# Kernel tuning notes

Hardware: AMD Instinct MI355X
Metric: run time of the kernel (lower is better)

## Reference

```python
import jax, jax.numpy as jnp
import numpy as np

B, IN_DIM, OUT_DIM, N, H = 64, 2, 1, 512, 64
SEQ, HOR, K, NSUP = 12, 12, 2, 2
TOT = 1 + NSUP * K  # number of diffusion matrices (identity + K steps per support)


def _lin_init(key, fan_in, shape):
    return jax.random.normal(key, shape, jnp.float32) / np.sqrt(fan_in)


def setup_inputs() -> dict:
    key = jax.random.key(0)
    ks = jax.random.split(key, 16)
    inputs = jax.random.normal(ks[0], (B, IN_DIM, N, SEQ), jnp.float32)
    A = jax.random.uniform(ks[1], (NSUP, N, N), jnp.float32)
    supports = A / A.sum(axis=2, keepdims=True)  # row-normalized transition matrices
    params = {}
    i = 2
    for pre, in0 in (('e', IN_DIM), ('d', OUT_DIM)):
        for l in range(2):
            cin = (in0 if l == 0 else H) + H
            params[f'{pre}{l}_wg'] = _lin_init(ks[i], TOT * cin, (TOT * cin, 2 * H)); i += 1
            params[f'{pre}{l}_bg'] = jnp.zeros((2 * H,), jnp.float32)
            params[f'{pre}{l}_wc'] = _lin_init(ks[i], TOT * cin, (TOT * cin, H)); i += 1
            params[f'{pre}{l}_bc'] = jnp.zeros((H,), jnp.float32)
    params['proj_w'] = _lin_init(ks[i], H, (OUT_DIM, H))
    params['proj_b'] = jnp.zeros((OUT_DIM,), jnp.float32)
    return {'inputs': inputs, 'supports': supports, **params}


def _gconv(x, h, supports, W, b):
    # x: (B,Cx,N), h: (B,H,N) -> (B,Dout,N)
    z = jnp.concatenate([x, h], axis=1)
    feats = [z]
    for s in range(NSUP):
        xk = z
        for _ in range(K):
            xk = jnp.einsum('nm,bcm->bcn', supports[s], xk)
            feats.append(xk)
    zf = jnp.concatenate(feats, axis=1)  # (B, TOT*C, N)
    return jnp.einsum('bcn,cd->bdn', zf, W) + b[None, :, None]


def _cell(x, h, supports, wg, bg, wc, bc):
    ru = jax.nn.sigmoid(_gconv(x, h, supports, wg, bg))
    r, u = jnp.split(ru, 2, axis=1)
    c = jnp.tanh(_gconv(x, r * h, supports, wc, bc))
    return u * h + (1.0 - u) * c


def _run(inputs, supports, p):
    h0 = jnp.zeros((B, H, N), jnp.float32)
    h1 = jnp.zeros((B, H, N), jnp.float32)

    def enc_step(carry, x):
        h0, h1 = carry
        h0 = _cell(x, h0, supports, p['e0_wg'], p['e0_bg'], p['e0_wc'], p['e0_bc'])
        h1 = _cell(h0, h1, supports, p['e1_wg'], p['e1_bg'], p['e1_wc'], p['e1_bc'])
        return (h0, h1), None

    xs = jnp.moveaxis(inputs, -1, 0)  # (SEQ,B,IN_DIM,N)
    (h0, h1), _ = jax.lax.scan(enc_step, (h0, h1), xs)

    go = jnp.zeros((B, OUT_DIM, N), jnp.float32)

    def dec_step(carry, _):
        x, h0, h1 = carry
        h0 = _cell(x, h0, supports, p['d0_wg'], p['d0_bg'], p['d0_wc'], p['d0_bc'])
        h1 = _cell(h0, h1, supports, p['d1_wg'], p['d1_bg'], p['d1_wc'], p['d1_bc'])
        y = jnp.einsum('bhn,oh->bon', h1, p['proj_w']) + p['proj_b'][None, :, None]
        return (y, h0, h1), y

    _, ys = jax.lax.scan(dec_step, (go, h0, h1), None, length=HOR)
    return jnp.moveaxis(ys, 0, -1)  # (B, OUT_DIM, N, HOR)


def reference(inputs, supports, e0_wg, e0_bg, e0_wc, e0_bc, e1_wg, e1_bg, e1_wc, e1_bc,
              d0_wg, d0_bg, d0_wc, d0_bc, d1_wg, d1_bg, d1_wc, d1_bc, proj_w, proj_b):
    p = dict(e0_wg=e0_wg, e0_bg=e0_bg, e0_wc=e0_wc, e0_bc=e0_bc,
             e1_wg=e1_wg, e1_bg=e1_bg, e1_wc=e1_wc, e1_bc=e1_bc,
             d0_wg=d0_wg, d0_bg=d0_bg, d0_wc=d0_wc, d0_bc=d0_bc,
             d1_wg=d1_wg, d1_bg=d1_bg, d1_wc=d1_wc, d1_bc=d1_bc,
             proj_w=proj_w, proj_b=proj_b)
    return _run(inputs, supports, p)
```

## Files before the change

kernel.cpp:

```cpp
#include <hip/hip_runtime.h>

#define B_ 64
#define N_ 512

typedef __attribute__((ext_vector_type(8))) short bf8_t;
typedef __attribute__((ext_vector_type(16))) float f16_t;
typedef __attribute__((ext_vector_type(4))) float f4v_t;

#define MFMA32(a, b, c) __builtin_amdgcn_mfma_f32_32x32x16_bf16(a, b, c, 0, 0, 0)

__device__ __forceinline__ ushort f2bf(float x) {
  union { float f; unsigned u; } v; v.f = x;
  unsigned r = v.u + 0x7FFFu + ((v.u >> 16) & 1u);
  return (ushort)(r >> 16);
}
__device__ __forceinline__ float bf2f(ushort h) {
  union { unsigned u; float f; } v; v.u = ((unsigned)h) << 16;
  return v.f;
}

__device__ __forceinline__ void gld16(const ushort* g, ushort* l) {
  __builtin_amdgcn_global_load_lds(
      (const __attribute__((address_space(1))) unsigned int*)(uintptr_t)g,
      (__attribute__((address_space(3))) unsigned int*)(uintptr_t)l,
      16, 0, 0);
}

__device__ __forceinline__ int xcd_logical(int nwg) {
  int lin = blockIdx.x + gridDim.x * (blockIdx.y + gridDim.y * blockIdx.z);
  return (lin & 7) * (nwg >> 3) + (lin >> 3);
}

__device__ __forceinline__ int swz32(int r) { return (r >> 1) & 3; }

template <int ROWS, int THREADS>
__device__ __forceinline__ void stage_tile2(const ushort* g, int lda, int k0,
                                            ushort* l, int tid) {
  constexpr int RT = (ROWS * 32) / (THREADS * 8);
#pragma unroll
  for (int q = 0; q < RT; ++q) {
    int e  = q * THREADS * 8 + tid * 8;
    int r  = e >> 5;
    int c8 = (e >> 3) & 3;
    int g8 = c8 ^ swz32(r);
    gld16(g + (size_t)r * lda + k0 + g8 * 8, l + e);
  }
}

__device__ __forceinline__ void core128(
    const ushort* Ah, const ushort* Al, int lda,
    const ushort* Bh, const ushort* Bl, int ldb,
    int K, ushort* lds, f16_t acc[2][2]) {
  constexpr int TILE = 128 * 32;
  constexpr int SSZ  = 4 * TILE;
  const int tid = threadIdx.x, lane = tid & 63, wave = tid >> 6;
  const int ar = lane & 31, hb = lane >> 5;
  const int wm = wave >> 1, wn = wave & 1;

  auto stage = [&](int buf, int k0) {
    ushort* lb = lds + buf * SSZ;
    stage_tile2<128, 256>(Ah, lda, k0, lb, tid);
    stage_tile2<128, 256>(Al, lda, k0, lb + TILE, tid);
    stage_tile2<128, 256>(Bh, ldb, k0, lb + 2 * TILE, tid);
    stage_tile2<128, 256>(Bl, ldb, k0, lb + 3 * TILE, tid);
  };

  const int nc = K >> 5;
  stage(0, 0);
  int buf = 0;
  for (int c = 0; c < nc; ++c) {
    __syncthreads();
    if (c + 1 < nc) stage(buf ^ 1, (c + 1) << 5);
    const ushort* lb = lds + buf * SSZ;
#pragma unroll
    for (int ks = 0; ks < 2; ++ks) {
      bf8_t ah[2], al[2], bh[2], bl[2];
#pragma unroll
      for (int i = 0; i < 2; ++i) {
        int r = wm * 64 + 32 * i + ar;
        int c8 = (ks * 2 + hb) ^ swz32(r);
        ah[i] = *(const bf8_t*)(lb + r * 32 + c8 * 8);
        al[i] = *(const bf8_t*)(lb + TILE + r * 32 + c8 * 8);
      }
#pragma unroll
      for (int j = 0; j < 2; ++j) {
        int r = wn * 64 + 32 * j + ar;
        int c8 = (ks * 2 + hb) ^ swz32(r);
        bh[j] = *(const bf8_t*)(lb + 2 * TILE + r * 32 + c8 * 8);
        bl[j] = *(const bf8_t*)(lb + 3 * TILE + r * 32 + c8 * 8);
      }
#pragma unroll
      for (int i = 0; i < 2; ++i)
#pragma unroll
        for (int j = 0; j < 2; ++j) {
          acc[i][j] = MFMA32(ah[i], bh[j], acc[i][j]);
          acc[i][j] = MFMA32(ah[i], bl[j], acc[i][j]);
          acc[i][j] = MFMA32(al[i], bh[j], acc[i][j]);
        }
    }
    buf ^= 1;
  }
}

__device__ __forceinline__ void core128_1(
    const ushort* Ah, int lda,
    const ushort* Bh, int ldb,
    int K, ushort* lds, f16_t acc[2][2]) {
  constexpr int TILE = 128 * 32;
  constexpr int SSZ  = 2 * TILE;
  const int tid = threadIdx.x, lane = tid & 63, wave = tid >> 6;
  const int ar = lane & 31, hb = lane >> 5;
  const int wm = wave >> 1, wn = wave & 1;

  auto stage = [&](int buf, int k0) {
    ushort* lb = lds + buf * SSZ;
    stage_tile2<128, 256>(Ah, lda, k0, lb, tid);
    stage_tile2<128, 256>(Bh, ldb, k0, lb + TILE, tid);
  };

  const int nc = K >> 5;
  stage(0, 0);
  int buf = 0;
  for (int c = 0; c < nc; ++c) {
    __syncthreads();
    if (c + 1 < nc) stage(buf ^ 1, (c + 1) << 5);
    const ushort* lb = lds + buf * SSZ;
#pragma unroll
    for (int ks = 0; ks < 2; ++ks) {
      bf8_t ah[2], bh[2];
#pragma unroll
      for (int i = 0; i < 2; ++i) {
        int r = wm * 64 + 32 * i + ar;
        int c8 = (ks * 2 + hb) ^ swz32(r);
        ah[i] = *(const bf8_t*)(lb + r * 32 + c8 * 8);
      }
#pragma unroll
      for (int j = 0; j < 2; ++j) {
        int r = wn * 64 + 32 * j + ar;
        int c8 = (ks * 2 + hb) ^ swz32(r);
        bh[j] = *(const bf8_t*)(lb + TILE + r * 32 + c8 * 8);
      }
#pragma unroll
      for (int i = 0; i < 2; ++i)
#pragma unroll
        for (int j = 0; j < 2; ++j)
          acc[i][j] = MFMA32(ah[i], bh[j], acc[i][j]);
    }
    buf ^= 1;
  }
}

__device__ __forceinline__ int crow32(int r, int hb) {
  return (r & 3) + 8 * (r >> 2) + 4 * hb;
}

__global__ __launch_bounds__(256) void stb_k(const float* __restrict__ S,
                                             ushort* __restrict__ Bcat,
                                             ushort* __restrict__ STb) {
  __shared__ float tile[16][17];
  int s = blockIdx.z;
  int n0 = blockIdx.y * 16, m0 = blockIdx.x * 16;
  int tx = threadIdx.x & 15, ty = threadIdx.x >> 4;
  float v = S[(size_t)s * 262144 + (size_t)(n0 + ty) * 512 + m0 + tx];
  tile[ty][tx] = v;
  Bcat[(size_t)(n0 + ty) * 2048 + (size_t)(2 * s) * 512 + m0 + tx] = f2bf(v);
  __syncthreads();
  STb[(size_t)s * 262144 + (size_t)(m0 + ty) * 512 + n0 + tx] = f2bf(tile[tx][ty]);
}

__global__ __launch_bounds__(256) void ssqm_k(const ushort* __restrict__ Bc,
                                              const ushort* __restrict__ STb,
                                              ushort* __restrict__ Bout) {
  __shared__ __attribute__((aligned(16))) ushort lds[2 * 2 * 128 * 32];
  int tid = threadIdx.x, lane = tid & 63, wave = tid >> 6;
  int wm = wave >> 1, wn = wave & 1, ar = lane & 31, hb = lane >> 5;
  int a = blockIdx.x, bm = blockIdx.y, s = blockIdx.z;
  f16_t acc[2][2] = {};
  core128_1(Bc + (size_t)(a * 128) * 2048 + (size_t)(2 * s) * 512, 2048,
            STb + (size_t)s * 262144 + (size_t)(bm * 128) * 512, 512,
            512, lds, acc);
#pragma unroll
  for (int i = 0; i < 2; ++i)
#pragma unroll
    for (int j = 0; j < 2; ++j) {
      int m_ = bm * 128 + wn * 64 + 32 * j + ar;
#pragma unroll
      for (int r = 0; r < 16; ++r) {
        int n_ = a * 128 + wm * 64 + 32 * i + crow32(r, hb);
        Bout[(size_t)n_ * 2048 + (size_t)(2 * s + 1) * 512 + m_] = f2bf(acc[i][j][r]);
      }
    }
}

struct WSrc { const float* wg[4]; const float* wc[4]; };

__global__ __launch_bounds__(256) void wprep_all_k(WSrc src,
                                                   ushort* __restrict__ Wbuf) {
  int idx = blockIdx.x * 256 + threadIdx.x;
  if (idx >= 4 * 147456) return;
  int ci = idx / 147456, r = idx % 147456;
  int C = (ci == 0) ? 66 : (ci == 2) ? 65 : 128;
  const float* WG = src.wg[ci];
  const float* WC = src.wc[ci];
  ushort v;
  if (r < 32768) {
    int e = r & 16383, c = e & 127, d = e >> 7;
    float x = (c < C) ? WG[(size_t)c * 128 + d] : 0.f;
    ushort hh = f2bf(x);
    v = (r < 16384) ? hh : f2bf(x - bf2f(hh));
  } else if (r < 98304) {
    int e = r - 32768, c = e & 127, i = e >> 7;
    int t = 1 + (i >> 7), d = i & 127;
    v = (c < C) ? f2bf(WG[(size_t)(t * C + c) * 128 + d]) : (ushort)0;
  } else if (r < 114688) {
    int e = (r - 98304) & 8191, c = e & 127, d = e >> 7;
    float x = (c < C) ? WC[(size_t)c * 64 + d] : 0.f;
    ushort hh = f2bf(x);
    v = (r < 106496) ? hh : f2bf(x - bf2f(hh));
  } else {
    int e = r - 114688, c = e & 127, i = e >> 7;
    int t = 1 + (i >> 6), d = i & 63;
    v = (c < C) ? f2bf(WC[(size_t)(t * C + c) * 64 + d]) : (ushort)0;
  }
  Wbuf[idx] = v;
}

__global__ __launch_bounds__(256) void packzT_k(const float* __restrict__ xsrc,
                                                int xmode, int t, int Cx, int C,
                                                const float* __restrict__ hT,
                                                ushort* __restrict__ Zh,
                                                ushort* __restrict__ Zl) {
  int jg = blockIdx.x * 256 + threadIdx.x;
  int b = jg >> 9, n = jg & 511;
  for (int c0 = 0; c0 < 128; c0 += 8) {
    bf8_t vh, vl;
#pragma unroll
    for (int q = 0; q < 8; ++q) {
      int c = c0 + q;
      float v;
      if (c < Cx) {
        if (xmode == 0)      v = xsrc[((size_t)(b * Cx + c) * 512 + n) * 12 + t];
        else if (xmode == 1) v = xsrc[jg];
        else                 v = xsrc[(size_t)jg * 64 + c];
      } else if (c < C) {
        v = hT[(size_t)jg * 64 + (c - Cx)];
      } else {
        v = 0.f;
      }
      ushort hh = f2bf(v);
      vh[q] = (short)hh;
      vl[q] = (short)f2bf(v - bf2f(hh));
    }
    *(bf8_t*)(Zh + (size_t)jg * 128 + c0) = vh;
    *(bf8_t*)(Zl + (size_t)jg * 128 + c0) = vl;
  }
}

template <int MODE>
__global__ __launch_bounds__(256, 2) void g1_k(const ushort* __restrict__ Wih,
                                               const ushort* __restrict__ Wil,
                                               const ushort* __restrict__ Wd,
                                               const ushort* __restrict__ Zh,
                                               const ushort* __restrict__ Zl,
                                               ushort* __restrict__ Gh,
                                               float* __restrict__ G0T, int K) {
  __shared__ __attribute__((aligned(16))) ushort lds[2 * 4 * 128 * 32];
  constexpr int DR = (MODE == 0) ? 128 : 64;
  constexpr int NMT = (MODE == 0) ? 4 : 2;
  int tid = threadIdx.x, lane = tid & 63, wave = tid >> 6;
  int wm = wave >> 1, wn = wave & 1, ar = lane & 31, hb = lane >> 5;
  int L = xcd_logical(256 * (NMT + 1));
  int mt = L % (NMT + 1), nt = L / (NMT + 1);
  f16_t acc[2][2] = {};
  if (mt == NMT) {
    core128(Wih, Wil, 128,
            Zh + (size_t)nt * 128 * 128, Zl + (size_t)nt * 128 * 128, 128,
            K, lds, acc);
#pragma unroll
    for (int i = 0; i < 2; ++i)
#pragma unroll
      for (int j = 0; j < 2; ++j) {
        int jg = nt * 128 + wn * 64 + 32 * j + ar;
#pragma unroll
        for (int r = 0; r < 16; ++r) {
          int d = wm * 64 + 32 * i + crow32(r, hb);
          if (d >= DR) continue;
          G0T[(size_t)jg * DR + d] = acc[i][j][r];
        }
      }
  } else {
    core128_1(Wd + (size_t)mt * 128 * 128, 128,
              Zh + (size_t)nt * 128 * 128, 128,
              K, lds, acc);
#pragma unroll
    for (int i = 0; i < 2; ++i)
#pragma unroll
      for (int j = 0; j < 2; ++j) {
        int jg = nt * 128 + wn * 64 + 32 * j + ar;
        int b = jg >> 9, m = jg & 511;
#pragma unroll
        for (int r = 0; r < 16; ++r) {
          int ii = mt * 128 + wm * 64 + 32 * i + crow32(r, hb);
          int tt = ii / DR, d = ii % DR;
          Gh[((size_t)(b * DR + d)) * 2048 + (size_t)tt * 512 + m] = f2bf(acc[i][j][r]);
        }
      }
  }
}

__global__ __launch_bounds__(256, 3) void ru1g_k(const ushort* __restrict__ Gh,
                                                 const ushort* __restrict__ Bch,
                                                 float* __restrict__ P) {
  __shared__ __attribute__((aligned(16))) ushort lds[2 * 2 * 128 * 32];
  int tid = threadIdx.x, lane = tid & 63, wave = tid >> 6;
  int wm = wave >> 1, wn = wave & 1, ar = lane & 31, hb = lane >> 5;
  int L = xcd_logical(768);
  int mt = L & 3, nt = (L >> 2) & 63, kz = L >> 8;
  int k0 = kz * 768;
  int K  = (kz == 2) ? 512 : 768;
  f16_t acc[2][2] = {};
  core128_1(Bch + (size_t)mt * 128 * 2048 + k0, 2048,
            Gh + (size_t)nt * 128 * 2048 + k0, 2048,
            K, lds, acc);
  float* Pz = P + (size_t)kz * 4194304;
#pragma unroll
  for (int i = 0; i < 2; ++i)
#pragma unroll
    for (int j = 0; j < 2; ++j) {
      int R = nt * 128 + wn * 64 + 32 * j + ar;
      int b = R >> 7, d = R & 127;
#pragma unroll
      for (int r = 0; r < 16; ++r) {
        int node = mt * 128 + wm * 64 + 32 * i + crow32(r, hb);
        Pz[((size_t)b * 512 + node) * 128 + d] = acc[i][j][r];
      }
    }
}

__global__ __launch_bounds__(256) void ru1f_k(const float* __restrict__ P,
                                              const float* __restrict__ G0T,
                                              const float* __restrict__ bg,
                                              const float* __restrict__ hT,
                                              float* __restrict__ U,
                                              ushort* __restrict__ Zh,
                                              ushort* __restrict__ Zl, int Cx) {
  int i4 = blockIdx.x * 256 + threadIdx.x;
  if (i4 >= 1048576) return;
  int base = i4 * 4;
  int row = base >> 7, d = base & 127;
  f4v_t p0 = *(const f4v_t*)(P + base);
  f4v_t p1 = *(const f4v_t*)(P + 4194304 + base);
  f4v_t p2 = *(const f4v_t*)(P + 2 * 4194304 + base);
  f4v_t g0 = *(const f4v_t*)(G0T + base);
  if (d < 64) {
    f4v_t hv = *(const f4v_t*)(hT + (size_t)row * 64 + d);
#pragma unroll
    for (int e = 0; e < 4; ++e) {
      float s = 1.f / (1.f + expf(-(p0[e] + p1[e] + p2[e] + g0[e] + bg[d + e])));
      float rh = s * hv[e];
      ushort hh = f2bf(rh);
      Zh[(size_t)row * 128 + Cx + d + e] = hh;
      Zl[(size_t)row * 128 + Cx + d + e] = f2bf(rh - bf2f(hh));
    }
  } else {
    f4v_t uo;
#pragma unroll
    for (int e = 0; e < 4; ++e)
      uo[e] = 1.f / (1.f + expf(-(p0[e] + p1[e] + p2[e] + g0[e] + bg[d + e])));
    *(f4v_t*)(U + (size_t)row * 64 + (d - 64)) = uo;
  }
}

__global__ __launch_bounds__(256, 3) void ru2g_k(const ushort* __restrict__ Gh,
                                                 const ushort* __restrict__ Bch,
                                                 float* __restrict__ P) {
  __shared__ __attribute__((aligned(16))) ushort lds[2 * 2 * 128 * 32];
  int tid = threadIdx.x, lane = tid & 63, wave = tid >> 6;
  int wm = wave >> 1, wn = wave & 1, ar = lane & 31, hb = lane >> 5;
  int L = xcd_logical(512);
  int mt = L & 3, nt = (L >> 2) & 31, kz = L >> 7;
  f16_t acc[2][2] = {};
  core128_1(Bch + (size_t)mt * 128 * 2048 + kz * 512, 2048,
            Gh + (size_t)nt * 128 * 2048 + kz * 512, 2048,
            512, lds, acc);
  float* Pz = P + (size_t)kz * 2097152;
#pragma unroll
  for (int i = 0; i < 2; ++i)
#pragma unroll
    for (int j = 0; j < 2; ++j) {
      int R = nt * 128 + wn * 64 + 32 * j + ar;
      int b = R >> 6, d = R & 63;
#pragma unroll
      for (int r = 0; r < 16; ++r) {
        int node = mt * 128 + wm * 64 + 32 * i + crow32(r, hb);
        Pz[((size_t)b * 512 + node) * 64 + d] = acc[i][j][r];
      }
    }
}

__global__ __launch_bounds__(256) void ru2f_k(const float* __restrict__ P,
                                              const float* __restrict__ G0c,
                                              const float* __restrict__ bc,
                                              const float* __restrict__ U,
                                              float* __restrict__ hT) {
  int i4 = blockIdx.x * 256 + threadIdx.x;
  if (i4 >= 524288) return;
  int base = i4 * 4;
  int d = base & 63;
  f4v_t p0 = *(const f4v_t*)(P + base);
  f4v_t p1 = *(const f4v_t*)(P + 2097152 + base);
  f4v_t p2 = *(const f4v_t*)(P + 2 * 2097152 + base);
  f4v_t p3 = *(const f4v_t*)(P + 3 * 2097152 + base);
  f4v_t g0 = *(const f4v_t*)(G0c + base);
  f4v_t uv = *(const f4v_t*)(U + base);
  f4v_t hv = *(const f4v_t*)(hT + base);
#pragma unroll
  for (int e = 0; e < 4; ++e) {
    float ct = tanhf(p0[e] + p1[e] + p2[e] + p3[e] + g0[e] + bc[d + e]);
    hv[e] = uv[e] * hv[e] + (1.f - uv[e]) * ct;
  }
  *(f4v_t*)(hT + base) = hv;
}

__global__ __launch_bounds__(256) void proj_out_k(const float* __restrict__ h1T,
                                                  const float* __restrict__ pw,
                                                  const float* __restrict__ pb,
                                                  float* __restrict__ ybuf,
                                                  float* __restrict__ out, int k) {
  int idx = blockIdx.x * blockDim.x + threadIdx.x;
  if (idx >= B_ * N_) return;
  float s = pb[0];
  const float* hrow = h1T + (size_t)idx * 64;
#pragma unroll
  for (int j = 0; j < 64; ++j)
    s = fmaf(pw[j], hrow[j], s);
  ybuf[idx] = s;
  out[(size_t)idx * 12 + k] = s;
}

extern "C" void kernel_launch(void* const* d_in, const int* in_sizes, int n_in,
                              void* d_out, int out_size, void* d_ws, size_t ws_size,
                              hipStream_t stream) {
  const float* inputs   = (const float*)d_in[0];
  const float* supports = (const float*)d_in[1];
  WSrc wsrc;
  wsrc.wg[0] = (const float*)d_in[2];  wsrc.wg[1] = (const float*)d_in[6];
  wsrc.wg[2] = (const float*)d_in[10]; wsrc.wg[3] = (const float*)d_in[14];
  wsrc.wc[0] = (const float*)d_in[4];  wsrc.wc[1] = (const float*)d_in[8];
  wsrc.wc[2] = (const float*)d_in[12]; wsrc.wc[3] = (const float*)d_in[16];
  const float* Bg[4] = { (const float*)d_in[3],  (const float*)d_in[7],
                         (const float*)d_in[11], (const float*)d_in[15] };
  const float* Bc[4] = { (const float*)d_in[5],  (const float*)d_in[9],
                         (const float*)d_in[13], (const float*)d_in[17] };
  const float* proj_w = (const float*)d_in[18];
  const float* proj_b = (const float*)d_in[19];
  float* out = (float*)d_out;

  char* p = (char*)d_ws;
  auto carve = [&](size_t bytes) { void* q = p; p += (bytes + 255) & ~(size_t)255; return q; };
  ushort* Bch  = (ushort*)carve((size_t)512 * 2048 * 2);
  ushort* zTh  = (ushort*)carve((size_t)32768 * 128 * 2);
  ushort* zTl  = (ushort*)carve((size_t)32768 * 128 * 2);
  ushort* Gh   = (ushort*)carve((size_t)8192 * 2048 * 2);
  float*  G0T  = (float*)carve((size_t)32768 * 128 * 4);
  float*  P    = (float*)carve((size_t)3 * 4194304 * 4);
  float*  U    = (float*)carve((size_t)2097152 * 4);
  float*  h0   = (float*)carve((size_t)2097152 * 4);
  float*  h1   = (float*)carve((size_t)2097152 * 4);
  float*  ybuf = (float*)carve((size_t)B_ * N_ * 4);
  ushort* Wbuf = (ushort*)carve((size_t)4 * 147456 * 2);
  ushort* STb  = (ushort*)U;

  hipMemsetAsync(h0, 0, (size_t)2097152 * 4 * 2 + (size_t)B_ * N_ * 4, stream);

  stb_k<<<dim3(32, 32, 2), 256, 0, stream>>>(supports, Bch, STb);
  ssqm_k<<<dim3(4, 4, 2), 256, 0, stream>>>(Bch, STb, Bch);
  wprep_all_k<<<(4 * 147456 + 255) / 256, 256, 0, stream>>>(wsrc, Wbuf);

  auto cell = [&](int ci, int Cx, const float* x, int xmode, int t, float* h) {
    int C = Cx + 64;
    int K1 = (C + 31) & ~31;
    ushort* cw = Wbuf + (size_t)ci * 147456;
    ushort* Wgid_h = cw;          ushort* Wgid_l = cw + 16384;
    ushort* Wgd    = cw + 32768;
    ushort* Wcid_h = cw + 98304;  ushort* Wcid_l = cw + 106496;
    ushort* Wcd    = cw + 114688;
    packzT_k<<<128, 256, 0, stream>>>(x, xmode, t, Cx, C, h, zTh, zTl);
    g1_k<0><<<dim3(256, 5), 256, 0, stream>>>(Wgid_h, Wgid_l, Wgd, zTh, zTl, Gh, G0T, K1);
    ru1g_k<<<dim3(64, 4, 3), 256, 0, stream>>>(Gh, Bch, P);
    ru1f_k<<<4096, 256, 0, stream>>>(P, G0T, Bg[ci], h, U, zTh, zTl, Cx);
    g1_k<1><<<dim3(256, 3), 256, 0, stream>>>(Wcid_h, Wcid_l, Wcd, zTh, zTl, Gh, G0T, K1);
    ru2g_k<<<dim3(32, 4, 4), 256, 0, stream>>>(Gh, Bch, P);
    ru2f_k<<<2048, 256, 0, stream>>>(P, G0T, Bc[ci], U, h);
  };

  for (int t = 0; t < 12; ++t) {
    cell(0, 2, inputs, 0, t, h0);
    cell(1, 64, h0, 2, 0, h1);
  }
  for (int k = 0; k < 12; ++k) {
    cell(2, 1, ybuf, 1, 0, h0);
    cell(3, 64, h0, 2, 0, h1);
    proj_out_k<<<(B_ * N_ + 255) / 256, 256, 0, stream>>>(h1, proj_w, proj_b, ybuf, out, k);
  }
}
```

Measured before the change: 6.206 ms.

## Fuse diffusion GEMMs with gate epilogues, dropping split-K partial buffers

Replaces the split-K GEMMs (ru1g/ru2g), which wrote fp32 partial sums to a P buffer, and their separate elementwise finalize kernels with single fused kernels. Each fused kernel runs the full K=2048 reduction and applies sigmoid/tanh and the GRU update in the epilogue. The GEMM core is templated over tile shapes, and smaller tiles (64x128, 64x64) are used so 512 blocks still fill the GPU without split-K. This removes large partial-sum traffic and two launches per cell. In exchange each block runs a longer serial K loop, and the epilogue does scattered, uncoalesced fp32 loads and stores.

After: 6.500 ms. +4.7%, slower.

```diff
diff --git a/kernel.cpp b/kernel.cpp
--- a/kernel.cpp
+++ b/kernel.cpp
@@ -45,6 +45,10 @@
     int g8 = c8 ^ swz32(r);
     gld16(g + (size_t)r * lda + k0 + g8 * 8, l + e);
   }
+}
+
+__device__ __forceinline__ int crow32(int r, int hb) {
+  return (r & 3) + 8 * (r >> 2) + 4 * hb;
 }
 
 __device__ __forceinline__ void core128(
@@ -102,20 +106,22 @@
   }
 }
 
-__device__ __forceinline__ void core128_1(
+template <int BM, int BN>
+__device__ __forceinline__ void core2(
     const ushort* Ah, int lda,
     const ushort* Bh, int ldb,
-    int K, ushort* lds, f16_t acc[2][2]) {
-  constexpr int TILE = 128 * 32;
-  constexpr int SSZ  = 2 * TILE;
+    int K, ushort* lds, f16_t acc[BM / 64][BN / 64]) {
+  constexpr int TA = BM * 32;
+  constexpr int SSZ = (BM + BN) * 32;
+  constexpr int FI = BM / 64, FJ = BN / 64;
   const int tid = threadIdx.x, lane = tid & 63, wave = tid >> 6;
   const int ar = lane & 31, hb = lane >> 5;
   const int wm = wave >> 1, wn = wave & 1;
 
   auto stage = [&](int buf, int k0) {
     ushort* lb = lds + buf * SSZ;
-    stage_tile2<128, 256>(Ah, lda, k0, lb, tid);
-    stage_tile2<128, 256>(Bh, ldb, k0, lb + TILE, tid);
+    stage_tile2<BM, 256>(Ah, lda, k0, lb, tid);
+    stage_tile2<BN, 256>(Bh, ldb, k0, lb + TA, tid);
   };
 
   const int nc = K >> 5;
@@ -127,31 +133,27 @@
     const ushort* lb = lds + buf * SSZ;
 #pragma unroll
     for (int ks = 0; ks < 2; ++ks) {
-      bf8_t ah[2], bh[2];
-#pragma unroll
-      for (int i = 0; i < 2; ++i) {
-        int r = wm * 64 + 32 * i + ar;
+      bf8_t ah[FI], bh[FJ];
+#pragma unroll
+      for (int i = 0; i < FI; ++i) {
+        int r = wm * (BM / 2) + 32 * i + ar;
         int c8 = (ks * 2 + hb) ^ swz32(r);
         ah[i] = *(const bf8_t*)(lb + r * 32 + c8 * 8);
       }
 #pragma unroll
-      for (int j = 0; j < 2; ++j) {
-        int r = wn * 64 + 32 * j + ar;
+      for (int j = 0; j < FJ; ++j) {
+        int r = wn * (BN / 2) + 32 * j + ar;
         int c8 = (ks * 2 + hb) ^ swz32(r);
-        bh[j] = *(const bf8_t*)(lb + TILE + r * 32 + c8 * 8);
-      }
-#pragma unroll
-      for (int i = 0; i < 2; ++i)
-#pragma unroll
-        for (int j = 0; j < 2; ++j)
+        bh[j] = *(const bf8_t*)(lb + TA + r * 32 + c8 * 8);
+      }
+#pragma unroll
+      for (int i = 0; i < FI; ++i)
+#pragma unroll
+        for (int j = 0; j < FJ; ++j)
           acc[i][j] = MFMA32(ah[i], bh[j], acc[i][j]);
     }
     buf ^= 1;
   }
-}
-
-__device__ __forceinline__ int crow32(int r, int hb) {
-  return (r & 3) + 8 * (r >> 2) + 4 * hb;
 }
 
 __global__ __launch_bounds__(256) void stb_k(const float* __restrict__ S,
@@ -176,9 +178,9 @@
   int wm = wave >> 1, wn = wave & 1, ar = lane & 31, hb = lane >> 5;
   int a = blockIdx.x, bm = blockIdx.y, s = blockIdx.z;
   f16_t acc[2][2] = {};
-  core128_1(Bc + (size_t)(a * 128) * 2048 + (size_t)(2 * s) * 512, 2048,
-            STb + (size_t)s * 262144 + (size_t)(bm * 128) * 512, 512,
-            512, lds, acc);
+  core2<128, 128>(Bc + (size_t)(a * 128) * 2048 + (size_t)(2 * s) * 512, 2048,
+                  STb + (size_t)s * 262144 + (size_t)(bm * 128) * 512, 512,
+                  512, lds, acc);
 #pragma unroll
   for (int i = 0; i < 2; ++i)
 #pragma unroll
@@ -289,9 +291,9 @@
         }
       }
   } else {
-    core128_1(Wd + (size_t)mt * 128 * 128, 128,
-              Zh + (size_t)nt * 128 * 128, 128,
-              K, lds, acc);
+    core2<128, 128>(Wd + (size_t)mt * 128 * 128, 128,
+                    Zh + (size_t)nt * 128 * 128, 128,
+                    K, lds, acc);
 #pragma unroll
     for (int i = 0; i < 2; ++i)
 #pragma unroll
@@ -308,118 +310,71 @@
   }
 }
 
-__global__ __launch_bounds__(256, 3) void ru1g_k(const ushort* __restrict__ Gh,
-                                                 const ushort* __restrict__ Bch,
-                                                 float* __restrict__ P) {
-  __shared__ __attribute__((aligned(16))) ushort lds[2 * 2 * 128 * 32];
-  int tid = threadIdx.x, lane = tid & 63, wave = tid >> 6;
-  int wm = wave >> 1, wn = wave & 1, ar = lane & 31, hb = lane >> 5;
-  int L = xcd_logical(768);
-  int mt = L & 3, nt = (L >> 2) & 63, kz = L >> 8;
-  int k0 = kz * 768;
-  int K  = (kz == 2) ? 512 : 768;
-  f16_t acc[2][2] = {};
-  core128_1(Bch + (size_t)mt * 128 * 2048 + k0, 2048,
-            Gh + (size_t)nt * 128 * 2048 + k0, 2048,
-            K, lds, acc);
-  float* Pz = P + (size_t)kz * 4194304;
-#pragma unroll
-  for (int i = 0; i < 2; ++i)
-#pragma unroll
-    for (int j = 0; j < 2; ++j) {
-      int R = nt * 128 + wn * 64 + 32 * j + ar;
-      int b = R >> 7, d = R & 127;
-#pragma unroll
-      for (int r = 0; r < 16; ++r) {
-        int node = mt * 128 + wm * 64 + 32 * i + crow32(r, hb);
-        Pz[((size_t)b * 512 + node) * 128 + d] = acc[i][j][r];
-      }
-    }
-}
-
-__global__ __launch_bounds__(256) void ru1f_k(const float* __restrict__ P,
-                                              const float* __restrict__ G0T,
-                                              const float* __restrict__ bg,
-                                              const float* __restrict__ hT,
-                                              float* __restrict__ U,
-                                              ushort* __restrict__ Zh,
-                                              ushort* __restrict__ Zl, int Cx) {
-  int i4 = blockIdx.x * 256 + threadIdx.x;
-  if (i4 >= 1048576) return;
-  int base = i4 * 4;
-  int row = base >> 7, d = base & 127;
-  f4v_t p0 = *(const f4v_t*)(P + base);
-  f4v_t p1 = *(const f4v_t*)(P + 4194304 + base);
-  f4v_t p2 = *(const f4v_t*)(P + 2 * 4194304 + base);
-  f4v_t g0 = *(const f4v_t*)(G0T + base);
-  if (d < 64) {
-    f4v_t hv = *(const f4v_t*)(hT + (size_t)row * 64 + d);
-#pragma unroll
-    for (int e = 0; e < 4; ++e) {
-      float s = 1.f / (1.f + expf(-(p0[e] + p1[e] + p2[e] + g0[e] + bg[d + e])));
-      float rh = s * hv[e];
-      ushort hh = f2bf(rh);
-      Zh[(size_t)row * 128 + Cx + d + e] = hh;
-      Zl[(size_t)row * 128 + Cx + d + e] = f2bf(rh - bf2f(hh));
-    }
-  } else {
-    f4v_t uo;
-#pragma unroll
-    for (int e = 0; e < 4; ++e)
-      uo[e] = 1.f / (1.f + expf(-(p0[e] + p1[e] + p2[e] + g0[e] + bg[d + e])));
-    *(f4v_t*)(U + (size_t)row * 64 + (d - 64)) = uo;
-  }
-}
-
-__global__ __launch_bounds__(256, 3) void ru2g_k(const ushort* __restrict__ Gh,
-                                                 const ushort* __restrict__ Bch,
-                                                 float* __restrict__ P) {
-  __shared__ __attribute__((aligned(16))) ushort lds[2 * 2 * 128 * 32];
+__global__ __launch_bounds__(256, 2) void ru1fused_k(const ushort* __restrict__ Gh,
+                                                     const ushort* __restrict__ Bch,
+                                                     const float* __restrict__ G0T,
+                                                     const float* __restrict__ bg,
+                                                     const float* __restrict__ hT,
+                                                     float* __restrict__ U,
+                                                     ushort* __restrict__ Zh,
+                                                     ushort* __restrict__ Zl,
+                                                     int Cx) {
+  __shared__ __attribute__((aligned(16))) ushort lds[2 * (64 + 128) * 32];
   int tid = threadIdx.x, lane = tid & 63, wave = tid >> 6;
   int wm = wave >> 1, wn = wave & 1, ar = lane & 31, hb = lane >> 5;
   int L = xcd_logical(512);
-  int mt = L & 3, nt = (L >> 2) & 31, kz = L >> 7;
-  f16_t acc[2][2] = {};
-  core128_1(Bch + (size_t)mt * 128 * 2048 + kz * 512, 2048,
-            Gh + (size_t)nt * 128 * 2048 + kz * 512, 2048,
-            512, lds, acc);
-  float* Pz = P + (size_t)kz * 2097152;
-#pragma unroll
-  for (int i = 0; i < 2; ++i)
-#pragma unroll
-    for (int j = 0; j < 2; ++j) {
-      int R = nt * 128 + wn * 64 + 32 * j + ar;
-      int b = R >> 6, d = R & 63;
-#pragma unroll
-      for (int r = 0; r < 16; ++r) {
-        int node = mt * 128 + wm * 64 + 32 * i + crow32(r, hb);
-        Pz[((size_t)b * 512 + node) * 64 + d] = acc[i][j][r];
+  int mt = L & 7, nt = L >> 3;
+  f16_t acc[1][2] = {};
+  core2<64, 128>(Bch + (size_t)mt * 64 * 2048, 2048,
+                 Gh + (size_t)nt * 128 * 2048, 2048,
+                 2048, lds, acc);
+#pragma unroll
+  for (int j = 0; j < 2; ++j) {
+    int d = wn * 64 + 32 * j + ar;
+    float bgd = bg[d];
+#pragma unroll
+    for (int r = 0; r < 16; ++r) {
+      int node = mt * 64 + wm * 32 + crow32(r, hb);
+      size_t row = (size_t)nt * 512 + node;
+      float s = 1.f / (1.f + expf(-(acc[0][j][r] + G0T[row * 128 + d] + bgd)));
+      if (d < 64) {
+        float rh = s * hT[row * 64 + d];
+        ushort hh = f2bf(rh);
+        Zh[row * 128 + Cx + d] = hh;
+        Zl[row * 128 + Cx + d] = f2bf(rh - bf2f(hh));
+      } else {
+        U[row * 64 + (d - 64)] = s;
       }
     }
-}
-
-__global__ __launch_bounds__(256) void ru2f_k(const float* __restrict__ P,
-                                              const float* __restrict__ G0c,
-                                              const float* __restrict__ bc,
-                                              const float* __restrict__ U,
-                                              float* __restrict__ hT) {
-  int i4 = blockIdx.x * 256 + threadIdx.x;
-  if (i4 >= 524288) return;
-  int base = i4 * 4;
-  int d = base & 63;
-  f4v_t p0 = *(const f4v_t*)(P + base);
-  f4v_t p1 = *(const f4v_t*)(P + 2097152 + base);
-  f4v_t p2 = *(const f4v_t*)(P + 2 * 2097152 + base);
-  f4v_t p3 = *(const f4v_t*)(P + 3 * 2097152 + base);
-  f4v_t g0 = *(const f4v_t*)(G0c + base);
-  f4v_t uv = *(const f4v_t*)(U + base);
-  f4v_t hv = *(const f4v_t*)(hT + base);
-#pragma unroll
-  for (int e = 0; e < 4; ++e) {
-    float ct = tanhf(p0[e] + p1[e] + p2[e] + p3[e] + g0[e] + bc[d + e]);
-    hv[e] = uv[e] * hv[e] + (1.f - uv[e]) * ct;
-  }
-  *(f4v_t*)(hT + base) = hv;
+  }
+}
+
+__global__ __launch_bounds__(256, 2) void ru2fused_k(const ushort* __restrict__ Gh,
+                                                     const ushort* __restrict__ Bch,
+                                                     const float* __restrict__ G0c,
+                                                     const float* __restrict__ bc,
+                                                     const float* __restrict__ U,
+                                                     float* __restrict__ hT) {
+  __shared__ __attribute__((aligned(16))) ushort lds[2 * (64 + 64) * 32];
+  int tid = threadIdx.x, lane = tid & 63, wave = tid >> 6;
+  int wm = wave >> 1, wn = wave & 1, ar = lane & 31, hb = lane >> 5;
+  int L = xcd_logical(512);
+  int mt = L & 7, nt = L >> 3;
+  f16_t acc[1][1] = {};
+  core2<64, 64>(Bch + (size_t)mt * 64 * 2048, 2048,
+                Gh + (size_t)nt * 64 * 2048, 2048,
+                2048, lds, acc);
+  int d = wn * 32 + ar;
+  float bcd = bc[d];
+#pragma unroll
+  for (int r = 0; r < 16; ++r) {
+    int node = mt * 64 + wm * 32 + crow32(r, hb);
+    size_t row = (size_t)nt * 512 + node;
+    size_t ix = row * 64 + d;
+    float ct = tanhf(acc[0][0][r] + G0c[ix] + bcd);
+    float u = U[ix];
+    hT[ix] = u * hT[ix] + (1.f - u) * ct;
+  }
 }
 
 __global__ __launch_bounds__(256) void proj_out_k(const float* __restrict__ h1T,
@@ -463,7 +418,6 @@
   ushort* zTl  = (ushort*)carve((size_t)32768 * 128 * 2);
   ushort* Gh   = (ushort*)carve((size_t)8192 * 2048 * 2);
   float*  G0T  = (float*)carve((size_t)32768 * 128 * 4);
-  float*  P    = (float*)carve((size_t)3 * 4194304 * 4);
   float*  U    = (float*)carve((size_t)2097152 * 4);
   float*  h0   = (float*)carve((size_t)2097152 * 4);
   float*  h1   = (float*)carve((size_t)2097152 * 4);
@@ -487,11 +441,9 @@
     ushort* Wcd    = cw + 114688;
     packzT_k<<<128, 256, 0, stream>>>(x, xmode, t, Cx, C, h, zTh, zTl);
     g1_k<0><<<dim3(256, 5), 256, 0, stream>>>(Wgid_h, Wgid_l, Wgd, zTh, zTl, Gh, G0T, K1);
-    ru1g_k<<<dim3(64, 4, 3), 256, 0, stream>>>(Gh, Bch, P);
-    ru1f_k<<<4096, 256, 0, stream>>>(P, G0T, Bg[ci], h, U, zTh, zTl, Cx);
+    ru1fused_k<<<512, 256, 0, stream>>>(Gh, Bch, G0T, Bg[ci], h, U, zTh, zTl, Cx);
     g1_k<1><<<dim3(256, 3), 256, 0, stream>>>(Wcid_h, Wcid_l, Wcd, zTh, zTl, Gh, G0T, K1);
-    ru2g_k<<<dim3(32, 4, 4), 256, 0, stream>>>(Gh, Bch, P);
-    ru2f_k<<<2048, 256, 0, stream>>>(P, G0T, Bc[ci], U, h);
+    ru2fused_k<<<512, 256, 0, stream>>>(Gh, Bch, G0T, Bc[ci], U, h);
   };
 
   for (int t = 0; t < 12; ++t) {
```
